# Optimization experiments

Hardware: AMD Instinct MI355X
Metric: run time of the kernel (lower is better)

## Reference

```python
import jax, jax.numpy as jnp
import numpy as np

NUM_HEADS = 8
GROUPS = 32  # min(32, 512 // 4)
EPS = 1e-5


def group_norm(y, gamma, beta):
    B, C, L = y.shape
    yg = y.reshape(B, GROUPS, -1)  # [B, G, (C//G)*L]
    mu = yg.mean(-1, keepdims=True)
    var = yg.var(-1, keepdims=True)
    yn = ((yg - mu) * jax.lax.rsqrt(var + EPS)).reshape(B, C, L)
    return yn * gamma[:, None] + beta[:, None]


def setup_inputs() -> dict:
    key = jax.random.key(0)
    ks = jax.random.split(key, 5)
    B, C, L = 4, 512, 2048
    return {
        "x": jax.random.normal(ks[0], (B, C, L), dtype=jnp.float32),
        "Wqkv": jax.random.normal(ks[1], (3 * C, C), dtype=jnp.float32) * (C ** -0.5),
        "bqkv": jax.random.normal(ks[2], (3 * C,), dtype=jnp.float32) * 0.01,
        "Wproj": jax.random.normal(ks[3], (C, C), dtype=jnp.float32) * (C ** -0.5),
        "bproj": jax.random.normal(ks[4], (C,), dtype=jnp.float32) * 0.01,
        "gamma": jnp.ones((C,), dtype=jnp.float32),
        "beta": jnp.zeros((C,), dtype=jnp.float32),
    }


def reference(x, Wqkv, bqkv, Wproj, bproj, gamma, beta):
    B, C, L = x.shape
    H = NUM_HEADS
    D = C // H
    # 1x1 Conv1d == channel-mixing matmul
    qkv = jnp.einsum('oc,bcl->bol', Wqkv, x) + bqkv[:, None]  # [B, 3C, L]
    qkv = qkv.reshape(B, 3, H, D, L)
    q, k, v = qkv[:, 0], qkv[:, 1], qkv[:, 2]
    q = jnp.clip(q, -10.0, 10.0)
    k = jnp.clip(k, -10.0, 10.0)
    v = jnp.clip(v, -10.0, 10.0)
    scale = D ** -0.5
    attn = jnp.einsum('bhdi,bhdj->bhij', q, k) * scale  # [B, H, L, L]
    attn = jnp.clip(attn, -10.0, 10.0)
    attn = jax.nn.softmax(attn, axis=-1)
    # NaN fallback: replace whole attn with identity if any NaN (matches torch branch)
    has_nan = jnp.isnan(attn).any()
    attn = jnp.where(has_nan, jnp.eye(L, dtype=x.dtype), attn)
    out = jnp.einsum('bhij,bhdj->bhdi', attn, v)  # [B, H, D, L]
    out = out.reshape(B, C, L)
    out = jnp.einsum('oc,bcl->bol', Wproj, out) + bproj[:, None]
    return group_norm(out + x, gamma, beta)
```

## Files before the change

kernel.cpp:

```cpp
#include <hip/hip_runtime.h>
#include <cstddef>

#define B_ 4
#define C_ 512
#define L_ 2048

typedef __attribute__((ext_vector_type(8))) short  short8;
typedef __attribute__((ext_vector_type(4))) float  f32x4;
typedef __attribute__((ext_vector_type(4))) unsigned short us4;

#define AS1 __attribute__((address_space(1)))
#define AS3 __attribute__((address_space(3)))

__device__ __forceinline__ float clip10(float v){ return fminf(fmaxf(v,-10.0f),10.0f); }

__device__ __forceinline__ unsigned short f2bf(float f){
  union { float f; unsigned u; } v; v.f = f;
  unsigned r = v.u + 0x7fffu + ((v.u >> 16) & 1u);
  return (unsigned short)(r >> 16);
}
__device__ __forceinline__ unsigned pk_tr(float lo, float hi){
  return __builtin_amdgcn_perm(__float_as_uint(hi), __float_as_uint(lo), 0x07060302u);
}
__device__ __forceinline__ float bf2f(unsigned short u){
  return __uint_as_float(((unsigned)u)<<16);
}
__device__ __forceinline__ void gl16(const void* g, void* l){
  __builtin_amdgcn_global_load_lds((const AS1 unsigned*)g, (AS3 unsigned*)l, 16, 0, 0);
}
__device__ __forceinline__ void drain_dma(){
  asm volatile("s_waitcnt vmcnt(0)" ::: "memory");
}
__device__ __forceinline__ short8 mk8(unsigned a, unsigned b, unsigned c, unsigned d){
  union { unsigned u[4]; short8 s; } v;
  v.u[0]=a; v.u[1]=b; v.u[2]=c; v.u[3]=d;
  return v.s;
}

__global__ __launch_bounds__(256) void prep_k(
    const float* __restrict__ x, const float* __restrict__ Wq,
    const float* __restrict__ Wp, unsigned short* __restrict__ xT,
    unsigned short* __restrict__ Wqb, unsigned short* __restrict__ Wpb,
    float* __restrict__ part)
{
  const int blk = blockIdx.x;
  const int t = threadIdx.x;
  if (blk < 4096){
    __shared__ float tile[32][33];
    const int b = blk>>10, rem = blk&1023;
    const int c0 = (rem>>6)*32, l0 = (rem&63)*32;
    const int cr = t>>3, lc = (t&7)*4;
    const float4 v = *(const float4*)(x + ((size_t)b*C_ + c0+cr)*L_ + l0 + lc);
    tile[cr][lc]=v.x; tile[cr][lc+1]=v.y; tile[cr][lc+2]=v.z; tile[cr][lc+3]=v.w;
    __syncthreads();
    const int lr = t>>3, cc = (t&7)*4;
    const us4 o = { f2bf(tile[cc][lr]), f2bf(tile[cc+1][lr]),
                    f2bf(tile[cc+2][lr]), f2bf(tile[cc+3][lr]) };
    *(us4*)(xT + ((size_t)b*L_ + l0+lr)*C_ + c0 + cc) = o;
  } else if (blk < 5120){
    const int i = (blk-4096)*256 + t;
    const int NQ = 1536*512/4;
    const float* src; unsigned short* dst; int j;
    if (i < NQ){ src = Wq; dst = Wqb; j = i; }
    else       { src = Wp; dst = Wpb; j = i - NQ; }
    const float4 v = *(const float4*)(src + (size_t)j*4);
    const us4 o = { f2bf(v.x), f2bf(v.y), f2bf(v.z), f2bf(v.w) };
    *(us4*)(dst + (size_t)j*4) = o;
  } else {
    part[t] = 0.f;
  }
}

template<int MODE>
__global__ __launch_bounds__(256) void mfma_gemm(
    const unsigned short* __restrict__ Wb, const unsigned short* __restrict__ Bin,
    const float* __restrict__ bias, const float* __restrict__ xres,
    unsigned short* __restrict__ qT, unsigned short* __restrict__ kT,
    unsigned short* __restrict__ vN,
    float* __restrict__ part)
{
  __shared__ unsigned short SA[128*64];
  __shared__ unsigned short SB[128*64];
  const int t = threadIdx.x;
  const int b = blockIdx.z;
  const int mb = blockIdx.y, n0 = blockIdx.x*128, m0 = mb*128;
  const int lane = t&63, w = t>>6, wm = w>>1, wn = w&1;
  const int n = lane&15, q4 = lane>>4;
  const bool SWAP = (MODE==1) || (MODE==0 && mb>=8);

  f32x4 acc[4][4];
#pragma unroll
  for (int i=0;i<4;i++)
#pragma unroll
    for (int j=0;j<4;j++) acc[i][j] = (f32x4){0.f,0.f,0.f,0.f};

  const unsigned short* Arow = Wb + (size_t)m0*512;
  const unsigned short* Brow = Bin + ((size_t)b*L_ + n0)*512;

  for (int kt=0; kt<8; kt++){
    const int k0 = kt*64;
    __syncthreads();
#pragma unroll
    for (int i=0;i<4;i++){
      const int ch = t + 256*i;
      const int row = ch>>3, lc = (ch&7) ^ (row&7);
      gl16(Arow + (size_t)row*512 + k0 + lc*8, &SA[ch*8]);
      gl16(Brow + (size_t)row*512 + k0 + lc*8, &SB[ch*8]);
    }
    drain_dma();
    __syncthreads();
#pragma unroll
    for (int kk=0;kk<2;kk++){
      short8 aF[4], bF[4];
      const int pc = ((kk*4+q4) ^ (n&7))*8;
#pragma unroll
      for (int mt=0;mt<4;mt++) aF[mt] = *(const short8*)&SA[(wm*64+mt*16+n)*64 + pc];
#pragma unroll
      for (int nt=0;nt<4;nt++) bF[nt] = *(const short8*)&SB[(wn*64+nt*16+n)*64 + pc];
      if (SWAP){
#pragma unroll
        for (int mt=0;mt<4;mt++)
#pragma unroll
          for (int nt=0;nt<4;nt++)
            acc[mt][nt] = __builtin_amdgcn_mfma_f32_16x16x32_bf16(bF[nt], aF[mt], acc[mt][nt], 0,0,0);
      } else {
#pragma unroll
        for (int mt=0;mt<4;mt++)
#pragma unroll
          for (int nt=0;nt<4;nt++)
            acc[mt][nt] = __builtin_amdgcn_mfma_f32_16x16x32_bf16(aF[mt], bF[nt], acc[mt][nt], 0,0,0);
      }
    }
  }

  const float QS = 0.180336880f;
  if (MODE==0 && SWAP){
#pragma unroll
    for (int mt=0;mt<4;mt++){
      const int o = m0 + wm*64 + mt*16 + n;
      const float bv = bias[o];
#pragma unroll
      for (int nt=0;nt<4;nt++){
        const int p = ((nt>>1)<<2) | ((q4&1)<<3) | ((q4>>1)<<4) | ((nt&1)<<5);
        const int l = n0 + wn*64 + p;
        const float r0=clip10(acc[mt][nt][0]+bv), r1=clip10(acc[mt][nt][1]+bv),
                    r2=clip10(acc[mt][nt][2]+bv), r3=clip10(acc[mt][nt][3]+bv);
        const us4 ov = { f2bf(r0), f2bf(r1), f2bf(r2), f2bf(r3) };
        *(us4*)&vN[((size_t)b*512 + (o-1024))*L_ + l] = ov;
      }
    }
    return;
  }
  if (MODE==1){
#pragma unroll
    for (int mt=0;mt<4;mt++){
      const int o = m0 + wm*64 + mt*16 + n;
      const float bv = bias[o];
      float gs=0.f, gq=0.f;
#pragma unroll
      for (int nt=0;nt<4;nt++){
        const int l = n0 + wn*64 + nt*16 + q4*4;
        const float4 xv = *(const float4*)(xres + ((size_t)b*512 + o)*L_ + l);
        const float y0=acc[mt][nt][0]+bv+xv.x, y1=acc[mt][nt][1]+bv+xv.y,
                    y2=acc[mt][nt][2]+bv+xv.z, y3=acc[mt][nt][3]+bv+xv.w;
        gs += (y0+y1)+(y2+y3);
        gq += (y0*y0+y1*y1)+(y2*y2+y3*y3);
        const us4 ov = { f2bf(y0), f2bf(y1), f2bf(y2), f2bf(y3) };
        *(us4*)&vN[((size_t)b*512 + o)*L_ + l] = ov;
      }
#pragma unroll
      for (int off=1; off<64; off<<=1){
        gs += __shfl_xor(gs, off);
        gq += __shfl_xor(gq, off);
      }
      if (lane==0){
        const int g = mb*8 + wm*4 + mt;
        atomicAdd(&part[(b*32+g)*2+0], gs);
        atomicAdd(&part[(b*32+g)*2+1], gq);
      }
    }
    return;
  }
#pragma unroll
  for (int mt=0;mt<4;mt++){
    const int obase = m0 + wm*64 + mt*16 + q4*4;
    const float b0=bias[obase], b1=bias[obase+1], b2=bias[obase+2], b3=bias[obase+3];
#pragma unroll
    for (int nt=0;nt<4;nt++){
      const int l = n0 + wn*64 + nt*16 + n;
      float r0=clip10(acc[mt][nt][0]+b0), r1=clip10(acc[mt][nt][1]+b1),
            r2=clip10(acc[mt][nt][2]+b2), r3=clip10(acc[mt][nt][3]+b3);
      const int typ = mb>>2;
      const int oin = obase - typ*512;
      if (typ==0){ r0*=QS; r1*=QS; r2*=QS; r3*=QS; }
      unsigned short* dst = (typ==0) ? qT : kT;
      const us4 o = { f2bf(r0), f2bf(r1), f2bf(r2), f2bf(r3) };
      *(us4*)&dst[((size_t)b*L_ + l)*512 + oin] = o;
    }
  }
}

#define OPX 68
#define PPITCH 21

__global__ __launch_bounds__(1024,8) void attn_v15(
    const unsigned short* __restrict__ qT, const unsigned short* __restrict__ kT,
    const unsigned short* __restrict__ vN,
    unsigned short* __restrict__ attnT)
{
  __shared__ unsigned short smem[32768];
  const int t  = threadIdx.x;
  const int id  = blockIdx.x;
  const int xcd = id & 7, s = id >> 3;
  const int pr  = xcd*4 + (s & 3);
  const int i0  = (s >> 2) * 128;
  const int h   = pr & 7, b = pr >> 3;
  const int lane = t&63, w = t>>6, n = lane&15, q4 = lane>>4;
  const int iw = w & 7;
  const int jg = w >> 3;
  const int jbase = jg*1024;

  const unsigned short* kb0 = kT + (size_t)b*L_*512 + h*64;
  const unsigned short* vb  = vN + ((size_t)b*512 + h*64)*L_;

  short8 qf[2];
#pragma unroll
  for (int kk=0; kk<2; kk++)
    qf[kk] = *(const short8*)(qT + ((size_t)b*L_ + i0 + iw*16 + n)*512
                                 + h*64 + kk*32 + q4*8);

  short8 ones;
#pragma unroll
  for (int i=0;i<8;i++) ones[i] = (short)0x3F80;

  f32x4 oacc[4];
  f32x4 oden = (f32x4){0.f,0.f,0.f,0.f};
#pragma unroll
  for (int dt=0;dt<4;dt++) oacc[dt]=(f32x4){0.f,0.f,0.f,0.f};

  const float LIM = 14.4269504089f;

  const int tg = t & 511;
  const int srow = tg>>3, slc = (tg&7)^(srow&7);
  unsigned short* gbase = &smem[jg*16384];

  gl16(kb0 + (size_t)(jbase+srow)*512 + slc*8, &gbase[tg*8]);
  gl16(vb  + (size_t)srow*L_ + jbase  + slc*8, &gbase[4096 + tg*8]);
  drain_dma();
  __syncthreads();

  for (int jt=0; jt<16; jt++){
    const int cur = jt&1;
    const unsigned short* sk = &gbase[cur*8192];
    const unsigned short* sv = &gbase[cur*8192 + 4096];

    if (jt < 15){
      unsigned short* nb = &gbase[(cur^1)*8192];
      const int jn = jbase + (jt+1)*64;
      gl16(kb0 + (size_t)(jn+srow)*512 + slc*8, &nb[tg*8]);
      gl16(vb  + (size_t)srow*L_ + jn  + slc*8, &nb[4096 + tg*8]);
    }

    f32x4 sacc[4];
#pragma unroll
    for (int j4=0;j4<4;j4++) sacc[j4]=(f32x4){0.f,0.f,0.f,0.f};
#pragma unroll
    for (int kk=0;kk<2;kk++){
      const int pc = ((kk*4+q4) ^ (n&7))*8;
      short8 aK[4];
#pragma unroll
      for (int j4=0;j4<4;j4++) aK[j4] = *(const short8*)&sk[(j4*16+n)*64 + pc];
#pragma unroll
      for (int j4=0;j4<4;j4++)
        sacc[j4] = __builtin_amdgcn_mfma_f32_16x16x32_bf16(aK[j4], qf[kk], sacc[j4], 0,0,0);
    }

    unsigned pw[4][2];
#pragma unroll
    for (int j4=0;j4<4;j4++){
      const float e0 = __builtin_amdgcn_exp2f(__builtin_amdgcn_fmed3f(sacc[j4][0],-LIM,LIM));
      const float e1 = __builtin_amdgcn_exp2f(__builtin_amdgcn_fmed3f(sacc[j4][1],-LIM,LIM));
      const float e2 = __builtin_amdgcn_exp2f(__builtin_amdgcn_fmed3f(sacc[j4][2],-LIM,LIM));
      const float e3 = __builtin_amdgcn_exp2f(__builtin_amdgcn_fmed3f(sacc[j4][3],-LIM,LIM));
      pw[j4][0] = pk_tr(e0,e1);
      pw[j4][1] = pk_tr(e2,e3);
    }

#pragma unroll
    for (int kk=0;kk<2;kk++){
      const int pcv = ((kk*4+q4) ^ (n&7))*8;
      short8 bV[4];
#pragma unroll
      for (int dt=0;dt<4;dt++) bV[dt] = *(const short8*)&sv[(dt*16+n)*64 + pcv];
      const short8 pA = mk8(pw[kk][0], pw[kk][1], pw[kk+2][0], pw[kk+2][1]);
#pragma unroll
      for (int dt=0;dt<4;dt++)
        oacc[dt] = __builtin_amdgcn_mfma_f32_16x16x32_bf16(pA, bV[dt], oacc[dt], 0,0,0);
      oden = __builtin_amdgcn_mfma_f32_16x16x32_bf16(pA, ones, oden, 0,0,0);
    }
    drain_dma();
    __syncthreads();
  }

  float* pbuf = (float*)smem;
  if (jg == 1){
    const int slot = (iw*64 + lane)*PPITCH;
#pragma unroll
    for (int dt=0;dt<4;dt++)
#pragma unroll
      for (int r=0;r<4;r++) pbuf[slot + dt*4 + r] = oacc[dt][r];
#pragma unroll
    for (int r=0;r<4;r++) pbuf[slot + 16 + r] = oden[r];
  }
  __syncthreads();
  if (jg == 1) return;

  {
    const int slot = (iw*64 + lane)*PPITCH;
#pragma unroll
    for (int dt=0;dt<4;dt++)
#pragma unroll
      for (int r=0;r<4;r++) oacc[dt][r] += pbuf[slot + dt*4 + r];
#pragma unroll
    for (int r=0;r<4;r++) oden[r] += pbuf[slot + 16 + r];
  }

  float inv[4];
#pragma unroll
  for (int r=0;r<4;r++) inv[r] = 1.0f/oden[r];

  unsigned short* sb = &smem[21504];
#pragma unroll
  for (int dt=0;dt<4;dt++)
#pragma unroll
    for (int r=0;r<4;r++)
      sb[(iw*16 + q4*4 + r)*OPX + dt*16 + n] = f2bf(oacc[dt][r]*inv[r]);
#pragma unroll
  for (int it=0; it<4; it++){
    const int chunk = it*64 + lane;
    const int row = chunk>>4, c4 = (chunk&15)*4;
    const us4 ov = *(const us4*)&sb[(iw*16 + row)*OPX + c4];
    *(us4*)&attnT[((size_t)b*L_ + i0 + iw*16 + row)*512 + h*64 + c4] = ov;
  }
}

__global__ __launch_bounds__(256) void gn_apply(
    const unsigned short* __restrict__ yb, const float* __restrict__ part,
    const float* __restrict__ gamma, const float* __restrict__ beta,
    float* __restrict__ out)
{
  const int blk = blockIdx.x;
  const int b = blk>>7, g = (blk>>2)&31, s = blk&3;
  const float sum = part[(b*32+g)*2+0];
  const float sq  = part[(b*32+g)*2+1];
  const float mu = sum*(1.0f/32768.0f);
  const float rs = rsqrtf(sq*(1.0f/32768.0f) - mu*mu + 1e-5f);
  const size_t base = ((size_t)b*C_ + g*16)*L_ + s*512;
  const int t = threadIdx.x;
#pragma unroll
  for (int i=0;i<4;i++){
    const int chunk = i*256 + t;
    const int row = chunk>>6;
    const int lc  = (chunk&63)*8;
    const int c = g*16 + row;
    const float ga = gamma[c]*rs, be = beta[c] - mu*ga;
    const size_t off = base + (size_t)row*L_ + lc;
    const short8 v = *(const short8*)(yb + off);
    float4 r1, r2;
    r1.x = bf2f((unsigned short)v[0])*ga + be;
    r1.y = bf2f((unsigned short)v[1])*ga + be;
    r1.z = bf2f((unsigned short)v[2])*ga + be;
    r1.w = bf2f((unsigned short)v[3])*ga + be;
    r2.x = bf2f((unsigned short)v[4])*ga + be;
    r2.y = bf2f((unsigned short)v[5])*ga + be;
    r2.z = bf2f((unsigned short)v[6])*ga + be;
    r2.w = bf2f((unsigned short)v[7])*ga + be;
    *(float4*)(out+off)   = r1;
    *(float4*)(out+off+4) = r2;
  }
}

extern "C" void kernel_launch(void* const* d_in, const int* in_sizes, int n_in,
                              void* d_out, int out_size, void* d_ws, size_t ws_size,
                              hipStream_t stream)
{
  (void)in_sizes; (void)n_in; (void)out_size; (void)ws_size;
  const float* x     = (const float*)d_in[0];
  const float* Wqkv  = (const float*)d_in[1];
  const float* bqkv  = (const float*)d_in[2];
  const float* Wproj = (const float*)d_in[3];
  const float* bproj = (const float*)d_in[4];
  const float* gamma = (const float*)d_in[5];
  const float* beta  = (const float*)d_in[6];
  float* out = (float*)d_out;
  char* ws = (char*)d_ws;

  const size_t MB = 1024*1024;
  unsigned short* qT    = (unsigned short*)(ws);
  unsigned short* kT    = (unsigned short*)(ws +  8*MB);
  unsigned short* vN    = (unsigned short*)(ws + 16*MB);
  unsigned short* attnT = (unsigned short*)(ws + 24*MB);
  unsigned short* xT    = (unsigned short*)(ws + 32*MB);
  unsigned short* Wqb   = (unsigned short*)(ws + 42*MB);
  unsigned short* Wpb   = (unsigned short*)(ws + 44*MB);
  unsigned short* yb    = (unsigned short*)(ws + 45*MB);
  float*          part  = (float*)        (ws + 61*MB);

  prep_k      <<<dim3(5121),   256,0,stream>>>(x, Wqkv, Wproj, xT, Wqb, Wpb, part);
  mfma_gemm<0><<<dim3(16,12,4),256,0,stream>>>(Wqb, xT,    bqkv , nullptr, qT,kT,vN, nullptr);
  attn_v15    <<<dim3(512),   1024,0,stream>>>(qT, kT, vN, attnT);
  mfma_gemm<1><<<dim3(16, 4,4),256,0,stream>>>(Wpb, attnT, bproj, x, nullptr,nullptr, yb, part);
  gn_apply    <<<dim3(512),    256,0,stream>>>(yb, part, gamma, beta, out);
}
```

Before: 174.7 us.

## Software-pipeline attention loop with triple buffering and drop split-K reduction

The attention kernel moves from 1024 threads, where two wave groups each covered half the keys and then merged partials through shared memory, to 512 threads where each wave walks all 32 key tiles. The loop is software-pipelined: QK^T for tile t is issued alongside PV for tile t-1, and the softmax exponentials are computed after the MFMAs, with a three-slot K/V ring buffer in LDS. This removes the cross-group reduction and lets MFMA work overlap the exp and load latency. In exchange each block does twice as many serial iterations with half the waves per block, so per-CU parallelism now depends on several blocks fitting per CU.

New measurement: 177.7 us. No clear change (+1.7%).

```diff
diff --git a/kernel.cpp b/kernel.cpp
--- a/kernel.cpp
+++ b/kernel.cpp
@@ -201,14 +201,13 @@
 }
 
 #define OPX 68
-#define PPITCH 21
-
-__global__ __launch_bounds__(1024,8) void attn_v15(
+
+__global__ __launch_bounds__(512,4) void attn_v16(
     const unsigned short* __restrict__ qT, const unsigned short* __restrict__ kT,
     const unsigned short* __restrict__ vN,
     unsigned short* __restrict__ attnT)
 {
-  __shared__ unsigned short smem[32768];
+  __shared__ unsigned short smem[24576];
   const int t  = threadIdx.x;
   const int id  = blockIdx.x;
   const int xcd = id & 7, s = id >> 3;
@@ -216,9 +215,6 @@
   const int i0  = (s >> 2) * 128;
   const int h   = pr & 7, b = pr >> 3;
   const int lane = t&63, w = t>>6, n = lane&15, q4 = lane>>4;
-  const int iw = w & 7;
-  const int jg = w >> 3;
-  const int jbase = jg*1024;
 
   const unsigned short* kb0 = kT + (size_t)b*L_*512 + h*64;
   const unsigned short* vb  = vN + ((size_t)b*512 + h*64)*L_;
@@ -226,7 +222,7 @@
   short8 qf[2];
 #pragma unroll
   for (int kk=0; kk<2; kk++)
-    qf[kk] = *(const short8*)(qT + ((size_t)b*L_ + i0 + iw*16 + n)*512
+    qf[kk] = *(const short8*)(qT + ((size_t)b*L_ + i0 + w*16 + n)*512
                                  + h*64 + kk*32 + q4*8);
 
   short8 ones;
@@ -239,28 +235,18 @@
   for (int dt=0;dt<4;dt++) oacc[dt]=(f32x4){0.f,0.f,0.f,0.f};
 
   const float LIM = 14.4269504089f;
-
-  const int tg = t & 511;
-  const int srow = tg>>3, slc = (tg&7)^(srow&7);
-  unsigned short* gbase = &smem[jg*16384];
-
-  gl16(kb0 + (size_t)(jbase+srow)*512 + slc*8, &gbase[tg*8]);
-  gl16(vb  + (size_t)srow*L_ + jbase  + slc*8, &gbase[4096 + tg*8]);
+  const int srow = t>>3, slc = (t&7)^(srow&7);
+
+  gl16(kb0 + (size_t)srow*512 + slc*8, &smem[t*8]);
+  gl16(vb  + (size_t)srow*L_  + slc*8, &smem[4096 + t*8]);
   drain_dma();
   __syncthreads();
 
-  for (int jt=0; jt<16; jt++){
-    const int cur = jt&1;
-    const unsigned short* sk = &gbase[cur*8192];
-    const unsigned short* sv = &gbase[cur*8192 + 4096];
-
-    if (jt < 15){
-      unsigned short* nb = &gbase[(cur^1)*8192];
-      const int jn = jbase + (jt+1)*64;
-      gl16(kb0 + (size_t)(jn+srow)*512 + slc*8, &nb[tg*8]);
-      gl16(vb  + (size_t)srow*L_ + jn  + slc*8, &nb[4096 + tg*8]);
-    }
-
+  gl16(kb0 + (size_t)(64+srow)*512 + slc*8, &smem[8192 + t*8]);
+  gl16(vb  + (size_t)srow*L_ + 64  + slc*8, &smem[8192+4096 + t*8]);
+
+  unsigned pw[4][2];
+  {
     f32x4 sacc[4];
 #pragma unroll
     for (int j4=0;j4<4;j4++) sacc[j4]=(f32x4){0.f,0.f,0.f,0.f};
@@ -269,13 +255,11 @@
       const int pc = ((kk*4+q4) ^ (n&7))*8;
       short8 aK[4];
 #pragma unroll
-      for (int j4=0;j4<4;j4++) aK[j4] = *(const short8*)&sk[(j4*16+n)*64 + pc];
+      for (int j4=0;j4<4;j4++) aK[j4] = *(const short8*)&smem[(j4*16+n)*64 + pc];
 #pragma unroll
       for (int j4=0;j4<4;j4++)
         sacc[j4] = __builtin_amdgcn_mfma_f32_16x16x32_bf16(aK[j4], qf[kk], sacc[j4], 0,0,0);
     }
-
-    unsigned pw[4][2];
 #pragma unroll
     for (int j4=0;j4<4;j4++){
       const float e0 = __builtin_amdgcn_exp2f(__builtin_amdgcn_fmed3f(sacc[j4][0],-LIM,LIM));
@@ -285,62 +269,97 @@
       pw[j4][0] = pk_tr(e0,e1);
       pw[j4][1] = pk_tr(e2,e3);
     }
+  }
+  drain_dma();
+  __syncthreads();
+
+  int bc = 1;
+  for (int tt=1; tt<32; tt++){
+    const unsigned short* Kc = &smem[bc*8192];
+    const int bp = (bc==0) ? 2 : bc-1;
+    const unsigned short* Vp = &smem[bp*8192 + 4096];
+    const int bn = (bc==2) ? 0 : bc+1;
+
+    if (tt < 31){
+      const int jn = (tt+1)*64;
+      gl16(kb0 + (size_t)(jn+srow)*512 + slc*8, &smem[bn*8192 + t*8]);
+      gl16(vb  + (size_t)srow*L_ + jn  + slc*8, &smem[bn*8192+4096 + t*8]);
+    }
+
+    f32x4 sacc[4];
+#pragma unroll
+    for (int j4=0;j4<4;j4++) sacc[j4]=(f32x4){0.f,0.f,0.f,0.f};
+#pragma unroll
+    for (int kk=0;kk<2;kk++){
+      const int pc = ((kk*4+q4) ^ (n&7))*8;
+      short8 aK[4];
+#pragma unroll
+      for (int j4=0;j4<4;j4++) aK[j4] = *(const short8*)&Kc[(j4*16+n)*64 + pc];
+#pragma unroll
+      for (int j4=0;j4<4;j4++)
+        sacc[j4] = __builtin_amdgcn_mfma_f32_16x16x32_bf16(aK[j4], qf[kk], sacc[j4], 0,0,0);
+    }
 
 #pragma unroll
     for (int kk=0;kk<2;kk++){
       const int pcv = ((kk*4+q4) ^ (n&7))*8;
       short8 bV[4];
 #pragma unroll
-      for (int dt=0;dt<4;dt++) bV[dt] = *(const short8*)&sv[(dt*16+n)*64 + pcv];
+      for (int dt=0;dt<4;dt++) bV[dt] = *(const short8*)&Vp[(dt*16+n)*64 + pcv];
       const short8 pA = mk8(pw[kk][0], pw[kk][1], pw[kk+2][0], pw[kk+2][1]);
 #pragma unroll
       for (int dt=0;dt<4;dt++)
         oacc[dt] = __builtin_amdgcn_mfma_f32_16x16x32_bf16(pA, bV[dt], oacc[dt], 0,0,0);
       oden = __builtin_amdgcn_mfma_f32_16x16x32_bf16(pA, ones, oden, 0,0,0);
     }
+
+#pragma unroll
+    for (int j4=0;j4<4;j4++){
+      const float e0 = __builtin_amdgcn_exp2f(__builtin_amdgcn_fmed3f(sacc[j4][0],-LIM,LIM));
+      const float e1 = __builtin_amdgcn_exp2f(__builtin_amdgcn_fmed3f(sacc[j4][1],-LIM,LIM));
+      const float e2 = __builtin_amdgcn_exp2f(__builtin_amdgcn_fmed3f(sacc[j4][2],-LIM,LIM));
+      const float e3 = __builtin_amdgcn_exp2f(__builtin_amdgcn_fmed3f(sacc[j4][3],-LIM,LIM));
+      pw[j4][0] = pk_tr(e0,e1);
+      pw[j4][1] = pk_tr(e2,e3);
+    }
+
     drain_dma();
     __syncthreads();
-  }
-
-  float* pbuf = (float*)smem;
-  if (jg == 1){
-    const int slot = (iw*64 + lane)*PPITCH;
-#pragma unroll
-    for (int dt=0;dt<4;dt++)
-#pragma unroll
-      for (int r=0;r<4;r++) pbuf[slot + dt*4 + r] = oacc[dt][r];
-#pragma unroll
-    for (int r=0;r<4;r++) pbuf[slot + 16 + r] = oden[r];
-  }
-  __syncthreads();
-  if (jg == 1) return;
+    bc = bn;
+  }
 
   {
-    const int slot = (iw*64 + lane)*PPITCH;
-#pragma unroll
-    for (int dt=0;dt<4;dt++)
-#pragma unroll
-      for (int r=0;r<4;r++) oacc[dt][r] += pbuf[slot + dt*4 + r];
-#pragma unroll
-    for (int r=0;r<4;r++) oden[r] += pbuf[slot + 16 + r];
+    const unsigned short* Vf = &smem[1*8192 + 4096];
+#pragma unroll
+    for (int kk=0;kk<2;kk++){
+      const int pcv = ((kk*4+q4) ^ (n&7))*8;
+      short8 bV[4];
+#pragma unroll
+      for (int dt=0;dt<4;dt++) bV[dt] = *(const short8*)&Vf[(dt*16+n)*64 + pcv];
+      const short8 pA = mk8(pw[kk][0], pw[kk][1], pw[kk+2][0], pw[kk+2][1]);
+#pragma unroll
+      for (int dt=0;dt<4;dt++)
+        oacc[dt] = __builtin_amdgcn_mfma_f32_16x16x32_bf16(pA, bV[dt], oacc[dt], 0,0,0);
+      oden = __builtin_amdgcn_mfma_f32_16x16x32_bf16(pA, ones, oden, 0,0,0);
+    }
   }
 
   float inv[4];
 #pragma unroll
   for (int r=0;r<4;r++) inv[r] = 1.0f/oden[r];
 
-  unsigned short* sb = &smem[21504];
+  unsigned short* sb = smem;
 #pragma unroll
   for (int dt=0;dt<4;dt++)
 #pragma unroll
     for (int r=0;r<4;r++)
-      sb[(iw*16 + q4*4 + r)*OPX + dt*16 + n] = f2bf(oacc[dt][r]*inv[r]);
+      sb[(w*16 + q4*4 + r)*OPX + dt*16 + n] = f2bf(oacc[dt][r]*inv[r]);
 #pragma unroll
   for (int it=0; it<4; it++){
     const int chunk = it*64 + lane;
     const int row = chunk>>4, c4 = (chunk&15)*4;
-    const us4 ov = *(const us4*)&sb[(iw*16 + row)*OPX + c4];
-    *(us4*)&attnT[((size_t)b*L_ + i0 + iw*16 + row)*512 + h*64 + c4] = ov;
+    const us4 ov = *(const us4*)&sb[(w*16 + row)*OPX + c4];
+    *(us4*)&attnT[((size_t)b*L_ + i0 + w*16 + row)*512 + h*64 + c4] = ov;
   }
 }
 
@@ -408,7 +427,7 @@
 
   prep_k      <<<dim3(5121),   256,0,stream>>>(x, Wqkv, Wproj, xT, Wqb, Wpb, part);
   mfma_gemm<0><<<dim3(16,12,4),256,0,stream>>>(Wqb, xT,    bqkv , nullptr, qT,kT,vN, nullptr);
-  attn_v15    <<<dim3(512),   1024,0,stream>>>(qT, kT, vN, attnT);
+  attn_v16    <<<dim3(512),    512,0,stream>>>(qT, kT, vN, attnT);
   mfma_gemm<1><<<dim3(16, 4,4),256,0,stream>>>(Wpb, attnT, bproj, x, nullptr,nullptr, yb, part);
   gn_apply    <<<dim3(512),    256,0,stream>>>(yb, part, gamma, beta, out);
 }
```
